# Performance work log

Hardware: AMD Instinct MI355X
Metric: run time of the kernel (lower is better)

The kernel has to match this reference:

```python
import jax, jax.numpy as jnp
import numpy as np

B, H, S, E, V = 1024, 512, 300, 512, 50257
NO, NA, NV, NOS = 36, 26, 26, 20


def setup_inputs() -> dict:
    key = jax.random.key(0)
    ks = jax.random.split(key, 24)
    n = lambda k, shape, s=1.0: jax.random.normal(k, shape, dtype=jnp.float32) * s
    W = 0.02  # param init scale
    return {
        "objects": n(ks[0], (B, NO, H)),
        "action": n(ks[1], (B, NA, H)),
        "video": n(ks[2], (B, NV, H)),
        "object_semantics": n(ks[3], (B, NOS, S)),
        "action_semantics": n(ks[4], (B, S)),
        "video_semantics": n(ks[5], (B, S)),
        "embed": n(ks[6], (B, E)),
        "h0": n(ks[7], (1, B, H)),
        "c0": n(ks[8], (1, B, H)),
        "W_w": n(ks[9], (H, H), W),
        "Uo_w": n(ks[10], (H, H), W), "bo": jnp.ones((H,), jnp.float32), "wo_w": n(ks[11], (H,), W),
        "Uos_w": n(ks[12], (H, S), W), "bos": jnp.ones((H,), jnp.float32), "wos_w": n(ks[13], (H,), W),
        "Um_w": n(ks[14], (H, H), W), "bm": jnp.ones((H,), jnp.float32), "wm_w": n(ks[15], (H,), W),
        "Uv_w": n(ks[16], (H, H), W), "bv": jnp.ones((H,), jnp.float32), "wv_w": n(ks[17], (H,), W),
        "vis_w": n(ks[18], (H, 3 * H), W), "vis_b": jnp.zeros((H,), jnp.float32),
        "sem_w": n(ks[19], (H, 3 * S), W), "sem_b": jnp.zeros((H,), jnp.float32),
        "W_ih": n(ks[20], (4 * H, 2 * H + E), W), "W_hh": n(ks[21], (4 * H, H), W),
        "b_ih": jnp.zeros((4 * H,), jnp.float32), "b_hh": jnp.zeros((4 * H,), jnp.float32),
        "to_word_w": n(ks[22], (E, H), W), "to_word_b": jnp.zeros((E,), jnp.float32),
        "logit_w": n(ks[23], (V, E), W), "logit_b": jnp.zeros((V,), jnp.float32),
    }


def _attn(Wh, U, b, w, feats):
    # Bahdanau additive attention: Wh [B,H], U [B,N,H], b [H], w [H], feats [B,N,D]
    scores = jnp.einsum('bnh,h->bn', jnp.tanh(Wh[:, None, :] + U + b), w)
    a = jax.nn.softmax(scores, axis=1)
    return jnp.einsum('bn,bnd->bd', a, feats)


def reference(objects, action, video, object_semantics, action_semantics, video_semantics,
              embed, h0, c0, W_w, Uo_w, bo, wo_w, Uos_w, bos, wos_w, Um_w, bm, wm_w,
              Uv_w, bv, wv_w, vis_w, vis_b, sem_w, sem_b, W_ih, W_hh, b_ih, b_hh,
              to_word_w, to_word_b, logit_w, logit_b):
    last_hidden = h0[0]                      # [B,H]
    Wh = last_hidden @ W_w.T                 # [B,H]
    attn_objects = _attn(Wh, objects @ Uo_w.T, bo, wo_w, objects)
    attn_motion = _attn(Wh, action @ Um_w.T, bm, wm_w, action)
    attn_video = _attn(Wh, video @ Uv_w.T, bv, wv_w, video)
    visual = jnp.concatenate([attn_video, attn_motion, attn_objects], axis=-1) @ vis_w.T + vis_b
    attn_objs = _attn(Wh, object_semantics @ Uos_w.T, bos, wos_w, object_semantics)
    sem = jnp.concatenate([attn_objs, action_semantics, video_semantics], axis=-1) @ sem_w.T + sem_b
    x = jnp.concatenate([visual, sem, embed], axis=-1)   # [B, 2H+E]
    # single LSTM step (seq_len=1, num_layers=1), torch gate order i,f,g,o
    gates = x @ W_ih.T + b_ih + last_hidden @ W_hh.T + b_hh
    i, f, g, o = jnp.split(gates, 4, axis=-1)
    c = jax.nn.sigmoid(f) * c0[0] + jax.nn.sigmoid(i) * jnp.tanh(g)
    h = jax.nn.sigmoid(o) * jnp.tanh(c)
    word = h @ to_word_w.T + to_word_b
    output_prob = jax.nn.log_softmax(word @ logit_w.T + logit_b, axis=1)  # [B,V]
    return (output_prob, h[None], c[None])
```

## Files before the change

kernel.cpp:

```cpp
#include <hip/hip_runtime.h>
#include <hip/hip_bf16.h>
#include <cstdint>
#include <cstddef>
#include <type_traits>

#define TPB 256

typedef __attribute__((ext_vector_type(8))) short short8;
typedef __attribute__((ext_vector_type(4))) float floatx4;

__device__ __forceinline__ float bfbits2f(short v) {
    union { unsigned u; float f; } t;
    t.u = ((unsigned)(unsigned short)v) << 16;
    return t.f;
}

__device__ __forceinline__ void store_c(float* C, size_t off, float v) { C[off] = v; }
__device__ __forceinline__ void store_c(__hip_bfloat16* C, size_t off, float v) { C[off] = __float2bfloat16(v); }

__device__ __forceinline__ void gload16(const __hip_bfloat16* g, __hip_bfloat16* l) {
    __builtin_amdgcn_global_load_lds(
        (const __attribute__((address_space(1))) void*)g,
        (__attribute__((address_space(3))) void*)l, 16, 0, 0);
}

template<bool ROWG>
__device__ __forceinline__ void stage_cvt(const float* __restrict__ Msrc, long ld,
                                          long rowlim, int klim,
                                          long tilebase, int k0,
                                          __hip_bfloat16* Ls, int c)
{
    const int r = c >> 2;
    const int q = (c & 3) ^ ((r >> 1) & 3);
    const long gr = tilebase + r;
    const int gc = k0 + q * 8;
    union { __hip_bfloat16 h[8]; uint4 u4; } t;
    const bool rowok = !ROWG || (gr < rowlim);
    if (rowok && gc + 8 <= klim) {
        const float* s = Msrc + gr * ld + gc;
        const float4 v0 = *(const float4*)s;
        const float4 v1 = *(const float4*)(s + 4);
        t.h[0] = __float2bfloat16(v0.x); t.h[1] = __float2bfloat16(v0.y);
        t.h[2] = __float2bfloat16(v0.z); t.h[3] = __float2bfloat16(v0.w);
        t.h[4] = __float2bfloat16(v1.x); t.h[5] = __float2bfloat16(v1.y);
        t.h[6] = __float2bfloat16(v1.z); t.h[7] = __float2bfloat16(v1.w);
    } else {
#pragma unroll
        for (int e = 0; e < 8; ++e) {
            const float v = (rowok && (gc + e) < klim) ? Msrc[gr * ld + gc + e] : 0.f;
            t.h[e] = __float2bfloat16(v);
        }
    }
    *(uint4*)(&Ls[c * 8]) = t.u4;
}

template<typename TA, typename TB, typename OutT, bool ACC, bool BIAS, bool NEDGE, bool SWAPGRID, bool FUSE>
__global__ __launch_bounds__(TPB)
void gemm_bf(const TA* __restrict__ A, int lda, int Ka,
             const TB* __restrict__ Bm, int ldb, long NBrow,
             OutT* __restrict__ C, long ldc,
             const float* __restrict__ bias,
             int N, int K,
             float* __restrict__ rowsum)
{
    constexpr bool AF32 = std::is_same<TA, float>::value;
    constexpr bool BF32 = std::is_same<TB, float>::value;

    __shared__ __align__(16) __hip_bfloat16 As[128 * 32];
    __shared__ __align__(16) __hip_bfloat16 Bs[128 * 32];
    __shared__ float smrow[128];

    const int tid  = threadIdx.x;
    const int lane = tid & 63;
    const int wave = tid >> 6;
    const int wm   = (wave & 1) * 64;
    const int wn   = (wave >> 1) * 64;
    const int l15  = lane & 15;
    const int quad = lane >> 4;

    const unsigned gx = gridDim.x;
    const unsigned l  = blockIdx.y * gx + blockIdx.x;
    const unsigned nwg = gx * gridDim.y;
    const unsigned q8 = nwg >> 3, r8 = nwg & 7;
    const unsigned c8 = l & 7, i8 = l >> 3;
    const unsigned w  = (c8 < r8 ? c8 * (q8 + 1) : r8 * (q8 + 1) + (c8 - r8) * q8) + i8;
    const unsigned bx = w % gx, by = w / gx;
    const long tileM = (long)(SWAPGRID ? bx : by) * 128;
    const long tileN = (long)(SWAPGRID ? by : bx) * 128;

    const int c0 = tid, c1 = tid + 256;
    const int r0 = c0 >> 2, r1 = c1 >> 2;
    const int q0 = (c0 & 3) ^ ((r0 >> 1) & 3);
    const int q1 = (c1 & 3) ^ ((r1 >> 1) & 3);

    const __hip_bfloat16* a0 = nullptr; const __hip_bfloat16* a1 = nullptr;
    const __hip_bfloat16* b0 = nullptr; const __hip_bfloat16* b1 = nullptr;
    if constexpr (!AF32) {
        a0 = (const __hip_bfloat16*)A + (tileM + r0) * (long)lda + q0 * 8;
        a1 = (const __hip_bfloat16*)A + (tileM + r1) * (long)lda + q1 * 8;
    }
    if constexpr (!BF32) {
        b0 = (const __hip_bfloat16*)Bm + (tileN + r0) * (long)ldb + q0 * 8;
        b1 = (const __hip_bfloat16*)Bm + (tileN + r1) * (long)ldb + q1 * 8;
    }
    __hip_bfloat16* la0 = &As[c0 * 8];
    __hip_bfloat16* la1 = &As[c1 * 8];
    __hip_bfloat16* lb0 = &Bs[c0 * 8];
    __hip_bfloat16* lb1 = &Bs[c1 * 8];

    const int qs = quad ^ ((l15 >> 1) & 3);

    floatx4 acc[4][4];
#pragma unroll
    for (int i = 0; i < 4; ++i)
#pragma unroll
        for (int j = 0; j < 4; ++j)
            acc[i][j] = (floatx4){0.f, 0.f, 0.f, 0.f};

    for (int k0 = 0; k0 < K; k0 += 32) {
        if constexpr (!AF32) { gload16(a0, la0); gload16(a1, la1); a0 += 32; a1 += 32; }
        if constexpr (!BF32) { gload16(b0, lb0); gload16(b1, lb1); b0 += 32; b1 += 32; }
        if constexpr (AF32) {
            stage_cvt<false>((const float*)A, lda, 0, Ka, tileM, k0, As, c0);
            stage_cvt<false>((const float*)A, lda, 0, Ka, tileM, k0, As, c1);
        }
        if constexpr (BF32) {
            stage_cvt<true>((const float*)Bm, ldb, NBrow, K, tileN, k0, Bs, c0);
            stage_cvt<true>((const float*)Bm, ldb, NBrow, K, tileN, k0, Bs, c1);
        }
        __syncthreads();

        short8 af[4], bfg[4];
#pragma unroll
        for (int i = 0; i < 4; ++i)
            af[i] = *(const short8*)(&As[(wm + i * 16 + l15) * 32 + qs * 8]);
#pragma unroll
        for (int j = 0; j < 4; ++j)
            bfg[j] = *(const short8*)(&Bs[(wn + j * 16 + l15) * 32 + qs * 8]);
#pragma unroll
        for (int i = 0; i < 4; ++i)
#pragma unroll
            for (int j = 0; j < 4; ++j)
                acc[i][j] = __builtin_amdgcn_mfma_f32_16x16x32_bf16(af[i], bfg[j], acc[i][j], 0, 0, 0);
        __syncthreads();
    }

    if constexpr (FUSE) {
        for (int t = tid; t < 128; t += TPB) smrow[t] = 0.f;
        __syncthreads();
    }
#pragma unroll
    for (int i = 0; i < 4; ++i) {
        float es[4] = {0.f, 0.f, 0.f, 0.f};
#pragma unroll
        for (int j = 0; j < 4; ++j) {
            const long n = tileN + wn + j * 16 + l15;
            if (NEDGE && n >= N) continue;
            float bv = 0.f;
            if constexpr (BIAS) bv = bias[n];
#pragma unroll
            for (int r = 0; r < 4; ++r) {
                const long m = tileM + wm + i * 16 + quad * 4 + r;
                const size_t off = (size_t)(m * ldc + n);
                float v = acc[i][j][r] + bv;
                if constexpr (ACC) v += ((const float*)C)[off];
                store_c(C, off, v);
                if constexpr (FUSE) es[r] += __expf(v);
            }
        }
        if constexpr (FUSE) {
#pragma unroll
            for (int r = 0; r < 4; ++r)
                atomicAdd(&smrow[wm + i * 16 + quad * 4 + r], es[r]);
        }
    }
    if constexpr (FUSE) {
        __syncthreads();
        for (int t = tid; t < 128; t += TPB)
            atomicAdd(&rowsum[tileM + t], smrow[t]);
    }
}

union Bf4 { __hip_bfloat16 h[4]; uint2 u; };

__global__ __launch_bounds__(TPB)
void cvt2bf(const float* __restrict__ src, long sld,
            __hip_bfloat16* __restrict__ dst, long dld,
            int rows_dst, int cols_dst, int rows_src, int cols_src)
{
    const int idx = blockIdx.x * TPB + threadIdx.x;
    const int cpr = cols_dst >> 2;
    if (idx >= rows_dst * cpr) return;
    const int r  = idx / cpr;
    const int c4 = (idx - r * cpr) << 2;
    Bf4 o;
    if (r < rows_src && c4 + 4 <= cols_src) {
        const float4 v = *(const float4*)(src + (long)r * sld + c4);
        o.h[0] = __float2bfloat16(v.x); o.h[1] = __float2bfloat16(v.y);
        o.h[2] = __float2bfloat16(v.z); o.h[3] = __float2bfloat16(v.w);
    } else {
#pragma unroll
        for (int e = 0; e < 4; ++e) {
            const float v = (r < rows_src && (c4 + e) < cols_src)
                              ? src[(long)r * sld + c4 + e] : 0.f;
            o.h[e] = __float2bfloat16(v);
        }
    }
    *(uint2*)(dst + (long)r * dld + c4) = o.u;
}

__global__ __launch_bounds__(TPB)
void attn_kernel(const float* __restrict__ Wh,
                 const __hip_bfloat16* __restrict__ U,
                 const float* __restrict__ feats, int feats_ld,
                 const float* __restrict__ bias,
                 const float* __restrict__ w,
                 __hip_bfloat16* __restrict__ dst,
                 int dst_ld, int N, int D)
{
    const int b = blockIdx.x;
    const int tid = threadIdx.x;
    const int lane = tid & 63;
    const int wave = tid >> 6;
    __shared__ float sc[64];

    const float* whb = Wh + (size_t)b * 512;
    const int hoff = lane * 8;
    float wh[8], bb[8], ww[8];
    {
        float4 t0 = *(const float4*)(whb + hoff), t1 = *(const float4*)(whb + hoff + 4);
        wh[0]=t0.x; wh[1]=t0.y; wh[2]=t0.z; wh[3]=t0.w; wh[4]=t1.x; wh[5]=t1.y; wh[6]=t1.z; wh[7]=t1.w;
        t0 = *(const float4*)(bias + hoff); t1 = *(const float4*)(bias + hoff + 4);
        bb[0]=t0.x; bb[1]=t0.y; bb[2]=t0.z; bb[3]=t0.w; bb[4]=t1.x; bb[5]=t1.y; bb[6]=t1.z; bb[7]=t1.w;
        t0 = *(const float4*)(w + hoff); t1 = *(const float4*)(w + hoff + 4);
        ww[0]=t0.x; ww[1]=t0.y; ww[2]=t0.z; ww[3]=t0.w; ww[4]=t1.x; ww[5]=t1.y; ww[6]=t1.z; ww[7]=t1.w;
    }
    for (int n = wave; n < N; n += 4) {
        const short8 u = *(const short8*)(U + ((size_t)b * N + n) * 512 + hoff);
        float s = 0.f;
#pragma unroll
        for (int e = 0; e < 8; ++e)
            s += tanhf(wh[e] + bfbits2f(u[e]) + bb[e]) * ww[e];
#pragma unroll
        for (int off = 32; off > 0; off >>= 1) s += __shfl_down(s, off);
        if (lane == 0) sc[n] = s;
    }
    __syncthreads();
    if (tid == 0) {
        float mx = -3.4e38f;
        for (int n = 0; n < N; ++n) mx = fmaxf(mx, sc[n]);
        float sum = 0.f;
        for (int n = 0; n < N; ++n) { float e = expf(sc[n] - mx); sc[n] = e; sum += e; }
        const float inv = 1.f / sum;
        for (int n = 0; n < N; ++n) sc[n] *= inv;
    }
    __syncthreads();
    for (int d = tid; d < D; d += TPB) {
        float a = 0.f;
        for (int n = 0; n < N; ++n)
            a += sc[n] * feats[((size_t)b * N + n) * feats_ld + d];
        dst[(size_t)b * dst_ld + d] = __float2bfloat16(a);
    }
}

__device__ __forceinline__ float sigmoidf_(float x) { return 1.f / (1.f + expf(-x)); }

__global__ __launch_bounds__(TPB)
void lstm_kernel(const float* __restrict__ gates,
                 const float* __restrict__ b_ih,
                 const float* __restrict__ b_hh,
                 const float* __restrict__ c0,
                 float* __restrict__ out_h,
                 float* __restrict__ out_c,
                 __hip_bfloat16* __restrict__ h_bf,
                 float* __restrict__ rowsum)
{
    const int idx = blockIdx.x * TPB + threadIdx.x;
    if (idx >= 1024 * 512) return;
    if (idx < 1024) rowsum[idx] = 0.f;
    const int hh = idx & 511;
    const float* g = gates + (size_t)(idx >> 9) * 2048;
    const float gi = g[hh]        + b_ih[hh]        + b_hh[hh];
    const float gf = g[512 + hh]  + b_ih[512 + hh]  + b_hh[512 + hh];
    const float gg = g[1024 + hh] + b_ih[1024 + hh] + b_hh[1024 + hh];
    const float go = g[1536 + hh] + b_ih[1536 + hh] + b_hh[1536 + hh];
    const float c = sigmoidf_(gf) * c0[idx] + sigmoidf_(gi) * tanhf(gg);
    const float h = sigmoidf_(go) * tanhf(c);
    out_h[idx] = h;
    out_c[idx] = c;
    h_bf[idx]  = __float2bfloat16(h);
}

__global__ __launch_bounds__(TPB)
void lsub(float* __restrict__ logits, const float* __restrict__ rowsum, int V)
{
    const int b = blockIdx.y;
    float* row = logits + (size_t)b * V;
    const float lse = logf(rowsum[b]);
    const int tid = threadIdx.x;
    const int mis  = (int)(((uintptr_t)row >> 2) & 3);
    const int head = mis ? 4 - mis : 0;
    const int nv   = (V - head) >> 2;
    const int tail0 = head + nv * 4;
    if (blockIdx.x == 0) {
        if (tid < head) row[tid] -= lse;
        for (int i = tail0 + tid; i < V; i += TPB) row[i] -= lse;
    }
    for (int k = blockIdx.x * TPB + tid; k < nv; k += gridDim.x * TPB) {
        float4 x = *(const float4*)(row + head + 4 * k);
        x.x -= lse; x.y -= lse; x.z -= lse; x.w -= lse;
        *(float4*)(row + head + 4 * k) = x;
    }
}


extern "C" void kernel_launch(void* const* d_in, const int* in_sizes, int n_in,
                              void* d_out, int out_size, void* d_ws, size_t ws_size,
                              hipStream_t stream)
{
    (void)in_sizes; (void)n_in; (void)out_size; (void)ws_size;
    const int B = 1024, H = 512, S = 300, E = 512, V = 50257;
    const int NO = 36, NA = 26, NV_ = 26, NOS = 20;
    const int Sp = 320;
    const int S3p = 928;

    typedef const float* cf;
    cf objects   = (cf)d_in[0];
    cf action    = (cf)d_in[1];
    cf video     = (cf)d_in[2];
    cf obj_sem   = (cf)d_in[3];
    cf act_sem   = (cf)d_in[4];
    cf vid_sem   = (cf)d_in[5];
    cf embed     = (cf)d_in[6];
    cf h0        = (cf)d_in[7];
    cf c0        = (cf)d_in[8];
    cf W_w       = (cf)d_in[9];
    cf Uo_w      = (cf)d_in[10];
    cf bo        = (cf)d_in[11];
    cf wo_w      = (cf)d_in[12];
    cf Uos_w     = (cf)d_in[13];
    cf bos       = (cf)d_in[14];
    cf wos_w     = (cf)d_in[15];
    cf Um_w      = (cf)d_in[16];
    cf bm        = (cf)d_in[17];
    cf wm_w      = (cf)d_in[18];
    cf Uv_w      = (cf)d_in[19];
    cf bv        = (cf)d_in[20];
    cf wv_w      = (cf)d_in[21];
    cf vis_w     = (cf)d_in[22];
    cf vis_b     = (cf)d_in[23];
    cf sem_w     = (cf)d_in[24];
    cf sem_b     = (cf)d_in[25];
    cf W_ih      = (cf)d_in[26];
    cf W_hh      = (cf)d_in[27];
    cf b_ih      = (cf)d_in[28];
    cf b_hh      = (cf)d_in[29];
    cf to_word_w = (cf)d_in[30];
    cf to_word_b = (cf)d_in[31];
    cf logit_w   = (cf)d_in[32];
    cf logit_b   = (cf)d_in[33];

    typedef __hip_bfloat16 bf;
    char* p = (char*)d_ws;
    auto take = [&](size_t bytes) { char* r = p; p += (bytes + 255) & ~(size_t)255; return r; };

    float* Wh   = (float*)take((size_t)B * H * 4);
    bf* x       = (bf*)take((size_t)B * 2048 * 2);
    bf* xvis    = (bf*)take((size_t)B * 1536 * 2);
    bf* xsem    = (bf*)take((size_t)B * S3p * 2);
    bf* h_bf    = (bf*)take((size_t)B * H * 2);
    bf* word    = (bf*)take((size_t)B * E * 2);
    char* region = take((size_t)B * NO * H * 2);
    bf* U        = (bf*)region;
    float* gates = (float*)region;
    bf* Wcat     = (bf*)(region + (size_t)28 * 1024 * 1024);
    bf* wsm = (bf*)take((size_t)512 * 1536 * 2);
    float* rowsum = (float*)take((size_t)B * 4);

    float* out_logp = (float*)d_out;
    float* out_h = out_logp + (size_t)B * V;
    float* out_c = out_h + (size_t)B * H;

    const dim3 blk(TPB);
    auto g128 = [](int M, int N) { return dim3((unsigned)(N >> 7), (unsigned)(M >> 7)); };
    auto cvt = [&](const float* src, long sld, bf* dst, long dld,
                   int rd, int cd, int rs, int cs) {
        const int total = rd * (cd >> 2);
        cvt2bf<<<(total + TPB - 1) / TPB, blk, 0, stream>>>(src, sld, dst, dld, rd, cd, rs, cs);
    };

    cvt(h0, H, x + 1536, 2048, B, H, B, H);
    cvt(embed, E, x + 1024, 2048, B, E, B, E);
    cvt(act_sem, S, xsem + S, S3p, B, S, B, S);
    cvt(vid_sem, S, xsem + 2 * S, S3p, B, S, B, S);
    cvt(act_sem, S, xsem + 3 * S, S3p, B, S3p - 3 * S, 0, 0);

    cvt(W_w, H, wsm, H, H, H, H, H);
    gemm_bf<bf, bf, float, false, false, false, false, false><<<g128(B, H), blk, 0, stream>>>(
        x + 1536, 2048, H, wsm, H, 0, Wh, H, nullptr, H, H, nullptr);

    cvt(Uo_w, H, wsm, H, H, H, H, H);
    gemm_bf<float, bf, bf, false, false, false, false, false><<<g128(B * NO, H), blk, 0, stream>>>(
        objects, H, H, wsm, H, 0, U, H, nullptr, H, H, nullptr);
    attn_kernel<<<B, blk, 0, stream>>>(Wh, U, objects, H, bo, wo_w, xvis + 2 * H, 1536, NO, H);

    cvt(Um_w, H, wsm, H, H, H, H, H);
    gemm_bf<float, bf, bf, false, false, false, false, false><<<g128(B * NA, H), blk, 0, stream>>>(
        action, H, H, wsm, H, 0, U, H, nullptr, H, H, nullptr);
    attn_kernel<<<B, blk, 0, stream>>>(Wh, U, action, H, bm, wm_w, xvis + H, 1536, NA, H);

    cvt(Uv_w, H, wsm, H, H, H, H, H);
    gemm_bf<float, bf, bf, false, false, false, false, false><<<g128(B * NV_, H), blk, 0, stream>>>(
        video, H, H, wsm, H, 0, U, H, nullptr, H, H, nullptr);
    attn_kernel<<<B, blk, 0, stream>>>(Wh, U, video, H, bv, wv_w, xvis, 1536, NV_, H);

    cvt(Uos_w, S, wsm, Sp, H, Sp, H, S);
    gemm_bf<float, bf, bf, false, false, false, false, false><<<g128(B * NOS, H), blk, 0, stream>>>(
        obj_sem, S, S, wsm, Sp, 0, U, H, nullptr, H, Sp, nullptr);
    attn_kernel<<<B, blk, 0, stream>>>(Wh, U, obj_sem, S, bos, wos_w, xsem, S3p, NOS, S);

    cvt(W_ih, 2 * H + E, Wcat, 2048, 2048, 1536, 2048, 1536);
    cvt(W_hh, H, Wcat + 1536, 2048, 2048, 512, 2048, 512);

    cvt(vis_w, 3 * H, wsm, 3 * H, H, 3 * H, H, 3 * H);
    gemm_bf<bf, bf, bf, false, true, false, false, false><<<g128(B, H), blk, 0, stream>>>(
        xvis, 1536, 1536, wsm, 1536, 0, x, 2048, vis_b, H, 1536, nullptr);

    cvt(sem_w, 3 * S, wsm, S3p, H, S3p, H, 3 * S);
    gemm_bf<bf, bf, bf, false, true, false, false, false><<<g128(B, H), blk, 0, stream>>>(
        xsem, S3p, S3p, wsm, S3p, 0, x + H, 2048, sem_b, H, S3p, nullptr);

    gemm_bf<bf, bf, float, false, false, false, false, false><<<g128(B, 2048), blk, 0, stream>>>(
        x, 2048, 2048, Wcat, 2048, 0, gates, 2048, nullptr, 2048, 2048, nullptr);

    lstm_kernel<<<(B * H) / TPB, blk, 0, stream>>>(gates, b_ih, b_hh, c0, out_h, out_c, h_bf, rowsum);

    cvt(to_word_w, H, wsm, H, E, H, E, H);
    gemm_bf<bf, bf, bf, false, true, false, false, false><<<g128(B, E), blk, 0, stream>>>(
        h_bf, H, H, wsm, H, 0, word, E, to_word_b, E, H, nullptr);

    gemm_bf<bf, float, float, false, true, true, true, true><<<dim3(B / 128, (V + 127) / 128), blk, 0, stream>>>(
        word, E, E, logit_w, E, V, out_logp, (long)V, logit_b, V, E, rowsum);

    lsub<<<dim3(4, B), blk, 0, stream>>>(out_logp, rowsum, V);
}
```

Measured before the change: 1.188 ms.

## Double-buffer GEMM LDS tiles, pre-convert logit weights, replace rowsum atomics with partials

The GEMM mainloop now uses two LDS buffers, so the next K-tile is fetched (async LDS load or register prefetch of fp32 data) while MFMAs run on the current tile. That halves the barriers per iteration. The fp32 logit weight matrix is converted once to padded bf16 in workspace when space allows, so the big vocab GEMM can use direct global-to-LDS loads. The fused exp-sum now uses wave shuffles and writes per-tile partials instead of shared and global atomics, and lsub reduces those partials. The cost is double the LDS per block, which may lower occupancy, plus an extra conversion pass over the 50257x512 weight every call.

```diff
diff --git a/kernel.cpp b/kernel.cpp
--- a/kernel.cpp
+++ b/kernel.cpp
@@ -25,33 +25,38 @@
 }
 
 template<bool ROWG>
-__device__ __forceinline__ void stage_cvt(const float* __restrict__ Msrc, long ld,
-                                          long rowlim, int klim,
-                                          long tilebase, int k0,
-                                          __hip_bfloat16* Ls, int c)
+__device__ __forceinline__ void load_chunk_f32(const float* __restrict__ M, long ld,
+                                               long rowlim, int klim,
+                                               long tilebase, int k0, int c,
+                                               float4& lo, float4& hi)
 {
     const int r = c >> 2;
     const int q = (c & 3) ^ ((r >> 1) & 3);
     const long gr = tilebase + r;
     const int gc = k0 + q * 8;
-    union { __hip_bfloat16 h[8]; uint4 u4; } t;
     const bool rowok = !ROWG || (gr < rowlim);
     if (rowok && gc + 8 <= klim) {
-        const float* s = Msrc + gr * ld + gc;
-        const float4 v0 = *(const float4*)s;
-        const float4 v1 = *(const float4*)(s + 4);
-        t.h[0] = __float2bfloat16(v0.x); t.h[1] = __float2bfloat16(v0.y);
-        t.h[2] = __float2bfloat16(v0.z); t.h[3] = __float2bfloat16(v0.w);
-        t.h[4] = __float2bfloat16(v1.x); t.h[5] = __float2bfloat16(v1.y);
-        t.h[6] = __float2bfloat16(v1.z); t.h[7] = __float2bfloat16(v1.w);
+        const float* s = M + gr * ld + gc;
+        lo = *(const float4*)s;
+        hi = *(const float4*)(s + 4);
     } else {
-#pragma unroll
-        for (int e = 0; e < 8; ++e) {
-            const float v = (rowok && (gc + e) < klim) ? Msrc[gr * ld + gc + e] : 0.f;
-            t.h[e] = __float2bfloat16(v);
-        }
-    }
-    *(uint4*)(&Ls[c * 8]) = t.u4;
+        float v[8];
+#pragma unroll
+        for (int e = 0; e < 8; ++e)
+            v[e] = (rowok && (gc + e) < klim) ? M[gr * ld + gc + e] : 0.f;
+        lo = (float4){v[0], v[1], v[2], v[3]};
+        hi = (float4){v[4], v[5], v[6], v[7]};
+    }
+}
+
+__device__ __forceinline__ void cvt_write8(__hip_bfloat16* Lbase, int c, float4 lo, float4 hi)
+{
+    union { __hip_bfloat16 h[8]; uint4 u4; } t;
+    t.h[0] = __float2bfloat16(lo.x); t.h[1] = __float2bfloat16(lo.y);
+    t.h[2] = __float2bfloat16(lo.z); t.h[3] = __float2bfloat16(lo.w);
+    t.h[4] = __float2bfloat16(hi.x); t.h[5] = __float2bfloat16(hi.y);
+    t.h[6] = __float2bfloat16(hi.z); t.h[7] = __float2bfloat16(hi.w);
+    *(uint4*)(&Lbase[c * 8]) = t.u4;
 }
 
 template<typename TA, typename TB, typename OutT, bool ACC, bool BIAS, bool NEDGE, bool SWAPGRID, bool FUSE>
@@ -61,14 +66,14 @@
              OutT* __restrict__ C, long ldc,
              const float* __restrict__ bias,
              int N, int K,
-             float* __restrict__ rowsum)
+             float* __restrict__ rowpart)
 {
     constexpr bool AF32 = std::is_same<TA, float>::value;
     constexpr bool BF32 = std::is_same<TB, float>::value;
 
-    __shared__ __align__(16) __hip_bfloat16 As[128 * 32];
-    __shared__ __align__(16) __hip_bfloat16 Bs[128 * 32];
-    __shared__ float smrow[128];
+    __shared__ __align__(16) __hip_bfloat16 As[2][128 * 32];
+    __shared__ __align__(16) __hip_bfloat16 Bs[2][128 * 32];
+    __shared__ float smrow[2][128];
 
     const int tid  = threadIdx.x;
     const int lane = tid & 63;
@@ -103,10 +108,8 @@
         b0 = (const __hip_bfloat16*)Bm + (tileN + r0) * (long)ldb + q0 * 8;
         b1 = (const __hip_bfloat16*)Bm + (tileN + r1) * (long)ldb + q1 * 8;
     }
-    __hip_bfloat16* la0 = &As[c0 * 8];
-    __hip_bfloat16* la1 = &As[c1 * 8];
-    __hip_bfloat16* lb0 = &Bs[c0 * 8];
-    __hip_bfloat16* lb1 = &Bs[c1 * 8];
+    const float* Af = (const float*)A;
+    const float* Bf = (const float*)Bm;
 
     const int qs = quad ^ ((l15 >> 1) & 3);
 
@@ -117,38 +120,66 @@
         for (int j = 0; j < 4; ++j)
             acc[i][j] = (floatx4){0.f, 0.f, 0.f, 0.f};
 
-    for (int k0 = 0; k0 < K; k0 += 32) {
-        if constexpr (!AF32) { gload16(a0, la0); gload16(a1, la1); a0 += 32; a1 += 32; }
-        if constexpr (!BF32) { gload16(b0, lb0); gload16(b1, lb1); b0 += 32; b1 += 32; }
-        if constexpr (AF32) {
-            stage_cvt<false>((const float*)A, lda, 0, Ka, tileM, k0, As, c0);
-            stage_cvt<false>((const float*)A, lda, 0, Ka, tileM, k0, As, c1);
-        }
-        if constexpr (BF32) {
-            stage_cvt<true>((const float*)Bm, ldb, NBrow, K, tileN, k0, Bs, c0);
-            stage_cvt<true>((const float*)Bm, ldb, NBrow, K, tileN, k0, Bs, c1);
-        }
-        __syncthreads();
-
+    auto compute = [&](int cb) {
         short8 af[4], bfg[4];
 #pragma unroll
         for (int i = 0; i < 4; ++i)
-            af[i] = *(const short8*)(&As[(wm + i * 16 + l15) * 32 + qs * 8]);
+            af[i] = *(const short8*)(&As[cb][(wm + i * 16 + l15) * 32 + qs * 8]);
 #pragma unroll
         for (int j = 0; j < 4; ++j)
-            bfg[j] = *(const short8*)(&Bs[(wn + j * 16 + l15) * 32 + qs * 8]);
+            bfg[j] = *(const short8*)(&Bs[cb][(wn + j * 16 + l15) * 32 + qs * 8]);
 #pragma unroll
         for (int i = 0; i < 4; ++i)
 #pragma unroll
             for (int j = 0; j < 4; ++j)
                 acc[i][j] = __builtin_amdgcn_mfma_f32_16x16x32_bf16(af[i], bfg[j], acc[i][j], 0, 0, 0);
+    };
+
+    const int nt = K >> 5;
+
+    if constexpr (!AF32) { gload16(a0, &As[0][c0 * 8]); gload16(a1, &As[0][c1 * 8]); }
+    else {
+        float4 lo0, hi0, lo1, hi1;
+        load_chunk_f32<false>(Af, lda, 0, Ka, tileM, 0, c0, lo0, hi0);
+        load_chunk_f32<false>(Af, lda, 0, Ka, tileM, 0, c1, lo1, hi1);
+        cvt_write8(As[0], c0, lo0, hi0);
+        cvt_write8(As[0], c1, lo1, hi1);
+    }
+    if constexpr (!BF32) { gload16(b0, &Bs[0][c0 * 8]); gload16(b1, &Bs[0][c1 * 8]); }
+    else {
+        float4 lo0, hi0, lo1, hi1;
+        load_chunk_f32<true>(Bf, ldb, NBrow, K, tileN, 0, c0, lo0, hi0);
+        load_chunk_f32<true>(Bf, ldb, NBrow, K, tileN, 0, c1, lo1, hi1);
+        cvt_write8(Bs[0], c0, lo0, hi0);
+        cvt_write8(Bs[0], c1, lo1, hi1);
+    }
+    __syncthreads();
+
+    int cur = 0;
+    for (int t = 0; t + 1 < nt; ++t) {
+        const int kn = (t + 1) << 5;
+        float4 xl0, xh0, xl1, xh1;
+        float4 yl0, yh0, yl1, yh1;
+        if constexpr (!AF32) { gload16(a0 + kn, &As[cur ^ 1][c0 * 8]); gload16(a1 + kn, &As[cur ^ 1][c1 * 8]); }
+        else {
+            load_chunk_f32<false>(Af, lda, 0, Ka, tileM, kn, c0, xl0, xh0);
+            load_chunk_f32<false>(Af, lda, 0, Ka, tileM, kn, c1, xl1, xh1);
+        }
+        if constexpr (!BF32) { gload16(b0 + kn, &Bs[cur ^ 1][c0 * 8]); gload16(b1 + kn, &Bs[cur ^ 1][c1 * 8]); }
+        else {
+            load_chunk_f32<true>(Bf, ldb, NBrow, K, tileN, kn, c0, yl0, yh0);
+            load_chunk_f32<true>(Bf, ldb, NBrow, K, tileN, kn, c1, yl1, yh1);
+        }
+
+        compute(cur);
+
+        if constexpr (AF32) { cvt_write8(As[cur ^ 1], c0, xl0, xh0); cvt_write8(As[cur ^ 1], c1, xl1, xh1); }
+        if constexpr (BF32) { cvt_write8(Bs[cur ^ 1], c0, yl0, yh0); cvt_write8(Bs[cur ^ 1], c1, yl1, yh1); }
         __syncthreads();
-    }
-
-    if constexpr (FUSE) {
-        for (int t = tid; t < 128; t += TPB) smrow[t] = 0.f;
-        __syncthreads();
-    }
+        cur ^= 1;
+    }
+    compute(cur);
+
 #pragma unroll
     for (int i = 0; i < 4; ++i) {
         float es[4] = {0.f, 0.f, 0.f, 0.f};
@@ -170,14 +201,22 @@
         }
         if constexpr (FUSE) {
 #pragma unroll
-            for (int r = 0; r < 4; ++r)
-                atomicAdd(&smrow[wm + i * 16 + quad * 4 + r], es[r]);
+            for (int r = 0; r < 4; ++r) {
+                float v = es[r];
+                v += __shfl_xor(v, 1);
+                v += __shfl_xor(v, 2);
+                v += __shfl_xor(v, 4);
+                v += __shfl_xor(v, 8);
+                if (l15 == 0) smrow[wave >> 1][wm + i * 16 + quad * 4 + r] = v;
+            }
         }
     }
     if constexpr (FUSE) {
         __syncthreads();
-        for (int t = tid; t < 128; t += TPB)
-            atomicAdd(&rowsum[tileM + t], smrow[t]);
+        if (tid < 128) {
+            const long Mtot = (long)(SWAPGRID ? gridDim.x : gridDim.y) * 128;
+            rowpart[(size_t)(tileN >> 7) * Mtot + tileM + tid] = smrow[0][tid] + smrow[1][tid];
+        }
     }
 }
 
@@ -272,12 +311,10 @@
                  const float* __restrict__ c0,
                  float* __restrict__ out_h,
                  float* __restrict__ out_c,
-                 __hip_bfloat16* __restrict__ h_bf,
-                 float* __restrict__ rowsum)
+                 __hip_bfloat16* __restrict__ h_bf)
 {
     const int idx = blockIdx.x * TPB + threadIdx.x;
     if (idx >= 1024 * 512) return;
-    if (idx < 1024) rowsum[idx] = 0.f;
     const int hh = idx & 511;
     const float* g = gates + (size_t)(idx >> 9) * 2048;
     const float gi = g[hh]        + b_ih[hh]        + b_hh[hh];
@@ -292,12 +329,23 @@
 }
 
 __global__ __launch_bounds__(TPB)
-void lsub(float* __restrict__ logits, const float* __restrict__ rowsum, int V)
+void lsub(float* __restrict__ logits, const float* __restrict__ rowpart,
+          int NT, int Mrow, int V)
 {
     const int b = blockIdx.y;
     float* row = logits + (size_t)b * V;
-    const float lse = logf(rowsum[b]);
     const int tid = threadIdx.x;
+
+    __shared__ float red[TPB];
+    float s = 0.f;
+    for (int j = tid; j < NT; j += TPB) s += rowpart[(size_t)j * Mrow + b];
+    red[tid] = s; __syncthreads();
+    for (int st = TPB / 2; st > 0; st >>= 1) {
+        if (tid < st) red[tid] += red[tid + st];
+        __syncthreads();
+    }
+    const float lse = logf(red[0]);
+
     const int mis  = (int)(((uintptr_t)row >> 2) & 3);
     const int head = mis ? 4 - mis : 0;
     const int nv   = (V - head) >> 2;
@@ -318,11 +366,13 @@
                               void* d_out, int out_size, void* d_ws, size_t ws_size,
                               hipStream_t stream)
 {
-    (void)in_sizes; (void)n_in; (void)out_size; (void)ws_size;
+    (void)in_sizes; (void)n_in; (void)out_size;
     const int B = 1024, H = 512, S = 300, E = 512, V = 50257;
     const int NO = 36, NA = 26, NV_ = 26, NOS = 20;
     const int Sp = 320;
     const int S3p = 928;
+    const int NT = (V + 127) / 128;
+    const int Vp = NT * 128;
 
     typedef const float* cf;
     cf objects   = (cf)d_in[0];
@@ -375,7 +425,12 @@
     float* gates = (float*)region;
     bf* Wcat     = (bf*)(region + (size_t)28 * 1024 * 1024);
     bf* wsm = (bf*)take((size_t)512 * 1536 * 2);
-    float* rowsum = (float*)take((size_t)B * 4);
+    float* rowpart = (float*)take((size_t)NT * B * 4);
+
+    const size_t lbf_bytes = (size_t)Vp * E * 2;
+    const size_t used = (size_t)(p - (char*)d_ws);
+    const bool have_lbf = ws_size >= used + lbf_bytes + 256;
+    bf* logit_bf = have_lbf ? (bf*)take(lbf_bytes) : nullptr;
 
     float* out_logp = (float*)d_out;
     float* out_h = out_logp + (size_t)B * V;
@@ -421,6 +476,7 @@
 
     cvt(W_ih, 2 * H + E, Wcat, 2048, 2048, 1536, 2048, 1536);
     cvt(W_hh, H, Wcat + 1536, 2048, 2048, 512, 2048, 512);
+    if (have_lbf) cvt(logit_w, E, logit_bf, E, Vp, E, V, E);
 
     cvt(vis_w, 3 * H, wsm, 3 * H, H, 3 * H, H, 3 * H);
     gemm_bf<bf, bf, bf, false, true, false, false, false><<<g128(B, H), blk, 0, stream>>>(
@@ -433,14 +489,19 @@
     gemm_bf<bf, bf, float, false, false, false, false, false><<<g128(B, 2048), blk, 0, stream>>>(
         x, 2048, 2048, Wcat, 2048, 0, gates, 2048, nullptr, 2048, 2048, nullptr);
 
-    lstm_kernel<<<(B * H) / TPB, blk, 0, stream>>>(gates, b_ih, b_hh, c0, out_h, out_c, h_bf, rowsum);
+    lstm_kernel<<<(B * H) / TPB, blk, 0, stream>>>(gates, b_ih, b_hh, c0, out_h, out_c, h_bf);
 
     cvt(to_word_w, H, wsm, H, E, H, E, H);
     gemm_bf<bf, bf, bf, false, true, false, false, false><<<g128(B, E), blk, 0, stream>>>(
         h_bf, H, H, wsm, H, 0, word, E, to_word_b, E, H, nullptr);
 
-    gemm_bf<bf, float, float, false, true, true, true, true><<<dim3(B / 128, (V + 127) / 128), blk, 0, stream>>>(
-        word, E, E, logit_w, E, V, out_logp, (long)V, logit_b, V, E, rowsum);
-
-    lsub<<<dim3(4, B), blk, 0, stream>>>(out_logp, rowsum, V);
-}
+    if (have_lbf) {
+        gemm_bf<bf, bf, float, false, true, true, true, true><<<dim3(B / 128, NT), blk, 0, stream>>>(
+            word, E, E, logit_bf, E, 0, out_logp, (long)V, logit_b, V, E, rowpart);
+    } else {
+        gemm_bf<bf, float, float, false, true, true, true, true><<<dim3(B / 128, NT), blk, 0, stream>>>(
+            word, E, E, logit_w, E, V, out_logp, (long)V, logit_b, V, E, rowpart);
+    }
+
+    lsub<<<dim3(4, B), blk, 0, stream>>>(out_logp, rowpart, NT, B, V);
+}
```

New measurement: 1.141 ms. 1.04x faster.
